# Optimization experiments

Hardware: AMD Instinct MI355X
Metric: run time of the kernel (lower is better)

The kernel has to match this reference:

```python
import jax, jax.numpy as jnp
import numpy as np

N_NODES = 100000
IN_DIM = 128
HID = 128
OUT = 64
N_EDGES = 1600000


def _glorot(key, shape):
    fan_in = shape[1]
    bound = 1.0 / np.sqrt(fan_in)
    return jax.random.uniform(key, shape, jnp.float32, -bound, bound)


def setup_inputs() -> dict:
    key = jax.random.key(0)
    ks = jax.random.split(key, 12)
    x = jax.random.normal(ks[0], (N_NODES, IN_DIM), jnp.float32)
    edge_index = jax.random.randint(ks[1], (2, N_EDGES), 0, N_NODES, jnp.int64)
    return {
        "x": x,
        "edge_index": edge_index,
        "lin_W": _glorot(ks[2], (HID, IN_DIM)),
        "lin_b": _glorot(ks[3], (1, HID))[0],
        "c1_Wl": _glorot(ks[4], (HID, HID)),
        "c1_bl": _glorot(ks[5], (1, HID))[0],
        "c1_Wr": _glorot(ks[6], (HID, HID)),
        "c2_Wl": _glorot(ks[7], (OUT, HID)),
        "c2_bl": _glorot(ks[8], (1, OUT))[0],
        "c2_Wr": _glorot(ks[9], (OUT, HID)),
    }


def _sage_conv(x, edge_index, Wl, bl, Wr):
    # PyG SAGEConv (aggr='mean'): out_i = Wl @ mean_{j in N(i)} x_j + bl + Wr @ x_i
    n = x.shape[0]
    src, dst = edge_index[0], edge_index[1]
    msg_sum = jax.ops.segment_sum(x[src], dst, num_segments=n)          # [N, d]
    deg = jax.ops.segment_sum(jnp.ones((src.shape[0],), x.dtype), dst,
                              num_segments=n)                            # [N]
    mean = msg_sum / jnp.maximum(deg, 1.0)[:, None]                      # zero-deg -> 0
    return mean @ Wl.T + bl + x @ Wr.T


def reference(x, edge_index, lin_W, lin_b, c1_Wl, c1_bl, c1_Wr, c2_Wl, c2_bl, c2_Wr):
    h = jax.nn.relu(x @ lin_W.T + lin_b)                                 # [N, HID]
    h = jax.nn.relu(_sage_conv(h, edge_index, c1_Wl, c1_bl, c1_Wr))      # [N, HID]
    h = _sage_conv(h, edge_index, c2_Wl, c2_bl, c2_Wr)                   # [N, OUT]
    return jax.nn.log_softmax(h, axis=1)
```

## Files before the change

kernel.cpp:

```cpp
#include <hip/hip_runtime.h>


#define KDIM 128
#define CH 4096
#define BSH 8
#define BCAP 8192

using bf16x8 = __attribute__((ext_vector_type(8))) short;
using f32x4  = __attribute__((ext_vector_type(4))) float;
using f32x2  = __attribute__((ext_vector_type(2))) float;

__device__ __forceinline__ unsigned short f2bf_u(float f) {
    unsigned u = __float_as_uint(f);
    u += 0x7fffu + ((u >> 16) & 1u);
    return (unsigned short)(u >> 16);
}
__device__ __forceinline__ unsigned packbf2(float a, float b) {
    return (unsigned)f2bf_u(a) | ((unsigned)f2bf_u(b) << 16);
}
__device__ __forceinline__ float bf2f(short s) {
    return __uint_as_float(((unsigned)(unsigned short)s) << 16);
}
__device__ __forceinline__ unsigned char f2fp8(float v) {
    return (unsigned char)(__builtin_amdgcn_cvt_pk_fp8_f32(v, v, 0, false) & 0xff);
}
__device__ __forceinline__ void fp8x4_acc2(unsigned uu, f32x2* a) {
    a[0] += __builtin_amdgcn_cvt_pk_f32_fp8(uu, false);
    a[1] += __builtin_amdgcn_cvt_pk_f32_fp8(uu, true);
}
__device__ __forceinline__ uint4 fp8x8_to_bf16x8(uint2 u) {
    f32x2 a0 = __builtin_amdgcn_cvt_pk_f32_fp8(u.x, false);
    f32x2 a1 = __builtin_amdgcn_cvt_pk_f32_fp8(u.x, true);
    f32x2 a2 = __builtin_amdgcn_cvt_pk_f32_fp8(u.y, false);
    f32x2 a3 = __builtin_amdgcn_cvt_pk_f32_fp8(u.y, true);
    uint4 o;
    o.x = packbf2(a0.x, a0.y); o.y = packbf2(a1.x, a1.y);
    o.z = packbf2(a2.x, a2.y); o.w = packbf2(a3.x, a3.y);
    return o;
}
__device__ __forceinline__ uint2 bf16x8_to_fp8x8(const short* p) {
    unsigned w0 = __builtin_amdgcn_cvt_pk_fp8_f32(bf2f(p[0]), bf2f(p[1]), 0, false);
    w0 = (unsigned)__builtin_amdgcn_cvt_pk_fp8_f32(bf2f(p[2]), bf2f(p[3]), (int)w0, true);
    unsigned w1 = __builtin_amdgcn_cvt_pk_fp8_f32(bf2f(p[4]), bf2f(p[5]), 0, false);
    w1 = (unsigned)__builtin_amdgcn_cvt_pk_fp8_f32(bf2f(p[6]), bf2f(p[7]), (int)w1, true);
    return uint2{w0, w1};
}

__device__ __forceinline__ void gload_lds16(const short* g, short* l) {
    __builtin_amdgcn_global_load_lds(
        (const __attribute__((address_space(1))) unsigned int*)g,
        (__attribute__((address_space(3))) unsigned int*)l, 16, 0, 0);
}

__global__ __launch_bounds__(256) void fused_front(
    const int* __restrict__ ei, int* __restrict__ hist, int E, int nwg, int NB,
    const float* __restrict__ Wc1l, const float* __restrict__ Wc1r,
    const float* __restrict__ Wc2l, const float* __restrict__ Wc2r,
    short* __restrict__ wp,
    const float* __restrict__ X, const float* __restrict__ Wlin,
    const float* __restrict__ bias, unsigned char* __restrict__ h1q, int N)
{
    __shared__ __attribute__((aligned(16))) short xa[64 * 136];
    const int bid = blockIdx.x;
    const int t = threadIdx.x;

    if (bid < nwg) {
        int* lh = (int*)xa;
        for (int b = t; b < NB; b += 256) lh[b] = 0;
        __syncthreads();
        const int e0 = bid * CH, e1 = min(E, e0 + CH);
        for (int e = e0 + t; e < e1; e += 256)
            atomicAdd(&lh[ei[E + e] >> BSH], 1);
        __syncthreads();
        for (int b = t; b < NB; b += 256) hist[b * nwg + bid] = lh[b];
        return;
    }
    if (bid < nwg + 192) {
        int idx = (bid - nwg) * 256 + t;
        const float* W; short* dst; int off, ncf;
        if (idx < 16384)      { W = Wc1l; dst = wp;         off = idx;         ncf = 8; }
        else if (idx < 32768) { W = Wc1r; dst = wp + 16384; off = idx - 16384; ncf = 8; }
        else if (idx < 40960) { W = Wc2l; dst = wp + 32768; off = idx - 32768; ncf = 4; }
        else                  { W = Wc2r; dst = wp + 40960; off = idx - 40960; ncf = 4; }
        int j    = off & 7;
        int lane = (off >> 3) & 63;
        int cf   = (off >> 9) & (ncf - 1);
        int ks   = off >> ((ncf == 8) ? 12 : 11);
        int m = cf * 16 + (lane & 15);
        int k = ks * 32 + ((lane >> 4) << 3) + j;
        dst[off] = (short)f2bf_u(W[m * KDIM + k]);
        return;
    }

    const int w = t >> 6, lane = t & 63;
    const int row0 = (bid - nwg - 192) * 64;
    const int cf0 = w * 2;

    bf16x8 bwA[4][2];
    #pragma unroll
    for (int ks = 0; ks < 4; ++ks)
        #pragma unroll
        for (int c = 0; c < 2; ++c) {
            const int m = (cf0 + c) * 16 + (lane & 15);
            const int kb = ks * 32 + ((lane >> 4) << 3);
            const float4 wa = *(const float4*)(Wlin + m * KDIM + kb);
            const float4 wb = *(const float4*)(Wlin + m * KDIM + kb + 4);
            bf16x8 r;
            r[0] = (short)f2bf_u(wa.x); r[1] = (short)f2bf_u(wa.y);
            r[2] = (short)f2bf_u(wa.z); r[3] = (short)f2bf_u(wa.w);
            r[4] = (short)f2bf_u(wb.x); r[5] = (short)f2bf_u(wb.y);
            r[6] = (short)f2bf_u(wb.z); r[7] = (short)f2bf_u(wb.w);
            bwA[ks][c] = r;
        }

    #pragma unroll
    for (int j = 0; j < 4; ++j) {
        const int sl = t + 256 * j;
        const int r = sl >> 4, s = sl & 15;
        const int gg = s ^ (r & 7);
        const int grow = min(row0 + r, N - 1);
        const float4 f0 = *(const float4*)(X + (long)grow * KDIM + gg * 8);
        const float4 f1 = *(const float4*)(X + (long)grow * KDIM + gg * 8 + 4);
        uint4 o;
        o.x = packbf2(f0.x, f0.y); o.y = packbf2(f0.z, f0.w);
        o.z = packbf2(f1.x, f1.y); o.w = packbf2(f1.z, f1.w);
        *(uint4*)(xa + r * KDIM + s * 8) = o;
    }

    f32x4 acc[4][2];
    #pragma unroll
    for (int c = 0; c < 2; ++c) {
        const float bv = bias[(cf0 + c) * 16 + (lane & 15)];
        #pragma unroll
        for (int rf = 0; rf < 4; ++rf)
            acc[rf][c] = f32x4{bv, bv, bv, bv};
    }

    __syncthreads();

    #pragma unroll
    for (int ks = 0; ks < 4; ++ks) {
        #pragma unroll
        for (int rf = 0; rf < 4; ++rf) {
            const int rl = rf * 16 + (lane & 15);
            const int s = (ks * 4 + (lane >> 4)) ^ (rl & 7);
            const bf16x8 a = *(const bf16x8*)(xa + rl * KDIM + s * 8);
            #pragma unroll
            for (int c = 0; c < 2; ++c)
                acc[rf][c] = __builtin_amdgcn_mfma_f32_16x16x32_bf16(
                    a, bwA[ks][c], acc[rf][c], 0, 0, 0);
        }
    }

    __syncthreads();
    #pragma unroll
    for (int rf = 0; rf < 4; ++rf)
        #pragma unroll
        for (int c = 0; c < 2; ++c)
            #pragma unroll
            for (int q = 0; q < 4; ++q) {
                const int r = rf * 16 + (lane >> 4) * 4 + q;
                const int col = (cf0 + c) * 16 + (lane & 15);
                xa[r * 136 + col] = (short)f2bf_u(fmaxf(acc[rf][c][q], 0.f));
            }
    __syncthreads();
    #pragma unroll
    for (int j = 0; j < 4; ++j) {
        const int sl = t + 256 * j;
        const int r = sl >> 4, ch = sl & 15;
        const int row = row0 + r;
        if (row < N)
            *(uint2*)(h1q + (long)row * KDIM + ch * 8) =
                bf16x8_to_fp8x8(xa + r * 136 + ch * 8);
    }
}


__global__ __launch_bounds__(256) void greduce(
    const int* __restrict__ in, int* __restrict__ bsum, int n)
{
    const int t = threadIdx.x;
    const int idx = blockIdx.x * 1024 + t * 4;
    int s = 0;
    if (idx + 4 <= n) {
        int4 a = *(const int4*)(in + idx);
        s = a.x + a.y + a.z + a.w;
    } else {
        #pragma unroll
        for (int k = 0; k < 4; ++k) if (idx + k < n) s += in[idx + k];
    }
    #pragma unroll
    for (int d = 1; d < 64; d <<= 1) s += __shfl_xor(s, d);
    __shared__ int ws[4];
    if ((t & 63) == 0) ws[t >> 6] = s;
    __syncthreads();
    if (t == 0) bsum[blockIdx.x] = ws[0] + ws[1] + ws[2] + ws[3];
}

__global__ __launch_bounds__(256) void scan_bsums(int* __restrict__ bsum, int nb)
{
    const int t = threadIdx.x;
    const int lane = t & 63, wid = t >> 6;
    int v = (t < nb) ? bsum[t] : 0;
    int incl = v;
    #pragma unroll
    for (int d = 1; d < 64; d <<= 1) {
        int u = __shfl_up(incl, d);
        if (lane >= d) incl += u;
    }
    __shared__ int ws[4];
    if (lane == 63) ws[wid] = incl;
    __syncthreads();
    int woff = 0;
    #pragma unroll
    for (int w = 0; w < 4; ++w) if (w < wid) woff += ws[w];
    const int excl = woff + incl - v;
    if (t <= nb) bsum[t] = excl;
}

__global__ __launch_bounds__(256) void gapply(
    int* __restrict__ io, const int* __restrict__ bsum, int n)
{
    const int t = threadIdx.x;
    const int lane = t & 63, wid = t >> 6;
    const int idx = blockIdx.x * 1024 + t * 4;
    int v[4] = {0, 0, 0, 0};
    if (idx + 4 <= n) {
        int4 a = *(const int4*)(io + idx);
        v[0] = a.x; v[1] = a.y; v[2] = a.z; v[3] = a.w;
    } else {
        #pragma unroll
        for (int k = 0; k < 4; ++k) if (idx + k < n) v[k] = io[idx + k];
    }
    const int sum = v[0] + v[1] + v[2] + v[3];
    int incl = sum;
    #pragma unroll
    for (int d = 1; d < 64; d <<= 1) {
        int u = __shfl_up(incl, d);
        if (lane >= d) incl += u;
    }
    __shared__ int ws[4];
    if (lane == 63) ws[wid] = incl;
    __syncthreads();
    int woff = 0;
    #pragma unroll
    for (int w = 0; w < 4; ++w) if (w < wid) woff += ws[w];
    int excl = bsum[blockIdx.x] + woff + (incl - sum);
    if (idx + 4 <= n) {
        int4 o;
        o.x = excl; o.y = excl + v[0]; o.z = excl + v[0] + v[1];
        o.w = excl + v[0] + v[1] + v[2];
        *(int4*)(io + idx) = o;
    } else {
        #pragma unroll
        for (int k = 0; k < 4; ++k) {
            if (idx + k < n) { io[idx + k] = excl; excl += v[k]; }
        }
    }
}

__global__ __launch_bounds__(256) void bin_scatter(
    const int* __restrict__ ei, const int* __restrict__ hist_s,
    unsigned* __restrict__ packed, int E, int nwg, int NB)
{
    __shared__ int lc[512];
    const int w = blockIdx.x, t = threadIdx.x;
    for (int b = t; b < NB; b += 256) lc[b] = hist_s[b * nwg + w];
    __syncthreads();
    const int e0 = w * CH, e1 = min(E, e0 + CH);
    for (int e = e0 + t; e < e1; e += 256) {
        const int src = ei[e];
        const int dst = ei[E + e];
        const int b = dst >> BSH;
        const int pos = atomicAdd(&lc[b], 1);
        packed[pos] = ((unsigned)(dst & 255) << 17) | (unsigned)src;
    }
}

__global__ __launch_bounds__(256) void bucket_sort(
    const unsigned* __restrict__ packed, const int* __restrict__ hist_s,
    int* __restrict__ offs, float* __restrict__ degf, int* __restrict__ perm,
    int E, int nwg, int NB, int N)
{
    __shared__ unsigned le[BCAP];
    __shared__ int lp[BCAP];
    __shared__ int lh[256], lx[256], lc[256];
    __shared__ int ws[4];
    const int b = blockIdx.x, t = threadIdx.x;
    const int bb = hist_s[b * nwg];
    const int be = (b + 1 < NB) ? hist_s[(b + 1) * nwg] : E;
    int cnt = be - bb;
    if (cnt > BCAP) cnt = BCAP;
    for (int i = t; i < cnt; i += 256) le[i] = packed[bb + i];
    lh[t] = 0;
    __syncthreads();
    for (int i = t; i < cnt; i += 256) atomicAdd(&lh[le[i] >> 17], 1);
    __syncthreads();
    const int lane = t & 63, wid = t >> 6;
    const int v = lh[t];
    int incl = v;
    #pragma unroll
    for (int d = 1; d < 64; d <<= 1) {
        int u = __shfl_up(incl, d);
        if (lane >= d) incl += u;
    }
    if (lane == 63) ws[wid] = incl;
    __syncthreads();
    int woff = 0;
    #pragma unroll
    for (int w = 0; w < 4; ++w) if (w < wid) woff += ws[w];
    const int excl = woff + incl - v;
    lx[t] = excl;
    lc[t] = excl;
    __syncthreads();
    for (int i = t; i < cnt; i += 256) {
        const unsigned p = le[i];
        const int pos = atomicAdd(&lc[p >> 17], 1);
        lp[pos] = (int)(p & 0x1FFFFu);
    }
    __syncthreads();
    for (int i = t; i < cnt; i += 256) perm[bb + i] = lp[i];
    const int node = (b << BSH) + t;
    if (node < N) {
        offs[node] = bb + lx[t];
        degf[node] = (float)v;
    }
    if (b == NB - 1 && t == 0) offs[N] = E;
}


__global__ __launch_bounds__(256) void gather_mean_128(
    const unsigned char* __restrict__ h1q, const int* __restrict__ offs,
    const int* __restrict__ perm, const float* __restrict__ degf,
    short* __restrict__ agg, int N)
{
    const int node = blockIdx.x * 16 + (threadIdx.x >> 4);
    if (node >= N) return;
    const int c = threadIdx.x & 15;
    const int b = offs[node], e = offs[node + 1];
    f32x2 acc2[4];
    #pragma unroll
    for (int q = 0; q < 4; ++q) acc2[q] = f32x2{0.f, 0.f};
    int i = b;
    for (; i + 4 <= e; i += 4) {
        const int s0 = perm[i],     s1 = perm[i + 1];
        const int s2 = perm[i + 2], s3 = perm[i + 3];
        const uint2 u0 = *(const uint2*)(h1q + (long)s0 * KDIM + c * 8);
        const uint2 u1 = *(const uint2*)(h1q + (long)s1 * KDIM + c * 8);
        const uint2 u2 = *(const uint2*)(h1q + (long)s2 * KDIM + c * 8);
        const uint2 u3 = *(const uint2*)(h1q + (long)s3 * KDIM + c * 8);
        fp8x4_acc2(u0.x, acc2 + 0);  fp8x4_acc2(u0.y, acc2 + 2);
        fp8x4_acc2(u1.x, acc2 + 0);  fp8x4_acc2(u1.y, acc2 + 2);
        fp8x4_acc2(u2.x, acc2 + 0);  fp8x4_acc2(u2.y, acc2 + 2);
        fp8x4_acc2(u3.x, acc2 + 0);  fp8x4_acc2(u3.y, acc2 + 2);
    }
    for (; i < e; ++i) {
        const uint2 u = *(const uint2*)(h1q + (long)perm[i] * KDIM + c * 8);
        fp8x4_acc2(u.x, acc2 + 0);  fp8x4_acc2(u.y, acc2 + 2);
    }
    const float inv = 1.f / fmaxf(degf[node], 1.f);
    uint4 o;
    o.x = packbf2(acc2[0].x * inv, acc2[0].y * inv);
    o.y = packbf2(acc2[1].x * inv, acc2[1].y * inv);
    o.z = packbf2(acc2[2].x * inv, acc2[2].y * inv);
    o.w = packbf2(acc2[3].x * inv, acc2[3].y * inv);
    *(uint4*)(agg + (long)node * KDIM + c * 8) = o;
}

__global__ __launch_bounds__(256) void gather_out(
    const unsigned char* __restrict__ g2q, const short* __restrict__ r2,
    const int* __restrict__ offs, const int* __restrict__ perm,
    const float* __restrict__ degf, float* __restrict__ out, int N)
{
    const int node = blockIdx.x * 32 + (threadIdx.x >> 3);
    if (node >= N) return;
    const int c = threadIdx.x & 7;
    const int b = offs[node], e = offs[node + 1];
    f32x2 acc2[4];
    #pragma unroll
    for (int q = 0; q < 4; ++q) acc2[q] = f32x2{0.f, 0.f};
    int i = b;
    for (; i + 4 <= e; i += 4) {
        const int s0 = perm[i],     s1 = perm[i + 1];
        const int s2 = perm[i + 2], s3 = perm[i + 3];
        const uint2 u0 = *(const uint2*)(g2q + (long)s0 * 64 + c * 8);
        const uint2 u1 = *(const uint2*)(g2q + (long)s1 * 64 + c * 8);
        const uint2 u2 = *(const uint2*)(g2q + (long)s2 * 64 + c * 8);
        const uint2 u3 = *(const uint2*)(g2q + (long)s3 * 64 + c * 8);
        fp8x4_acc2(u0.x, acc2 + 0);  fp8x4_acc2(u0.y, acc2 + 2);
        fp8x4_acc2(u1.x, acc2 + 0);  fp8x4_acc2(u1.y, acc2 + 2);
        fp8x4_acc2(u2.x, acc2 + 0);  fp8x4_acc2(u2.y, acc2 + 2);
        fp8x4_acc2(u3.x, acc2 + 0);  fp8x4_acc2(u3.y, acc2 + 2);
    }
    for (; i < e; ++i) {
        const uint2 u = *(const uint2*)(g2q + (long)perm[i] * 64 + c * 8);
        fp8x4_acc2(u.x, acc2 + 0);  fp8x4_acc2(u.y, acc2 + 2);
    }
    const float inv = 1.f / fmaxf(degf[node], 1.f);
    const bf16x8 rv = *(const bf16x8*)(r2 + (long)node * 64 + c * 8);
    float v[8];
    v[0] = acc2[0].x * inv + bf2f(rv[0]);
    v[1] = acc2[0].y * inv + bf2f(rv[1]);
    v[2] = acc2[1].x * inv + bf2f(rv[2]);
    v[3] = acc2[1].y * inv + bf2f(rv[3]);
    v[4] = acc2[2].x * inv + bf2f(rv[4]);
    v[5] = acc2[2].y * inv + bf2f(rv[5]);
    v[6] = acc2[3].x * inv + bf2f(rv[6]);
    v[7] = acc2[3].y * inv + bf2f(rv[7]);
    float m = v[0];
    #pragma unroll
    for (int q = 1; q < 8; ++q) m = fmaxf(m, v[q]);
    m = fmaxf(m, __shfl_xor(m, 1));
    m = fmaxf(m, __shfl_xor(m, 2));
    m = fmaxf(m, __shfl_xor(m, 4));
    float s = 0.f;
    #pragma unroll
    for (int q = 0; q < 8; ++q) s += __expf(v[q] - m);
    s += __shfl_xor(s, 1);
    s += __shfl_xor(s, 2);
    s += __shfl_xor(s, 4);
    const float L = m + __logf(s);
    float4 oa = make_float4(v[0] - L, v[1] - L, v[2] - L, v[3] - L);
    float4 ob = make_float4(v[4] - L, v[5] - L, v[6] - L, v[7] - L);
    *(float4*)(out + (long)node * 64 + c * 8) = oa;
    *(float4*)(out + (long)node * 64 + c * 8 + 4) = ob;
}

__global__ __launch_bounds__(256) void gemm_c1c2(
    const short* __restrict__ A, const unsigned char* __restrict__ h1q,
    const short* __restrict__ wpA, const short* __restrict__ wpB,
    const short* __restrict__ wpL2, const short* __restrict__ wpR2,
    const float* __restrict__ bias1, const float* __restrict__ bias2,
    unsigned char* __restrict__ g2q, short* __restrict__ r2, int N)
{
    __shared__ __attribute__((aligned(16))) short xa[64 * KDIM];
    __shared__ __attribute__((aligned(16))) short xb[64 * 136];

    const int t = threadIdx.x;
    const int w = t >> 6, lane = t & 63;
    const int row0 = blockIdx.x * 64;
    const int cf0 = w * 2;

    bf16x8 bwA[4][2], bwB[4][2];
    #pragma unroll
    for (int ks = 0; ks < 4; ++ks)
        #pragma unroll
        for (int c = 0; c < 2; ++c) {
            bwA[ks][c] = *(const bf16x8*)(wpA + (((ks * 8) + cf0 + c) * 64 + lane) * 8);
            bwB[ks][c] = *(const bf16x8*)(wpB + (((ks * 8) + cf0 + c) * 64 + lane) * 8);
        }

    #pragma unroll
    for (int ii = 0; ii < 4; ++ii) {
        const int i = w * 4 + ii;
        const int rl = i * 4 + (lane >> 4);
        const int grow = min(row0 + rl, N - 1);
        const int gs = (lane & 15) ^ (rl & 7);
        gload_lds16(A + (long)grow * KDIM + gs * 8, &xa[i * 512]);
    }
    #pragma unroll
    for (int j = 0; j < 4; ++j) {
        const int sl = t + 256 * j;
        const int r = sl >> 4, s = sl & 15;
        const int gg = s ^ (r & 7);
        const int grow = min(row0 + r, N - 1);
        const uint2 u = *(const uint2*)(h1q + (long)grow * KDIM + gg * 8);
        *(uint4*)(xb + r * KDIM + s * 8) = fp8x8_to_bf16x8(u);
    }

    f32x4 acc[4][2];
    #pragma unroll
    for (int c = 0; c < 2; ++c) {
        const float bv = bias1[(cf0 + c) * 16 + (lane & 15)];
        #pragma unroll
        for (int rf = 0; rf < 4; ++rf)
            acc[rf][c] = f32x4{bv, bv, bv, bv};
    }

    __syncthreads();

    #pragma unroll
    for (int ks = 0; ks < 4; ++ks) {
        #pragma unroll
        for (int rf = 0; rf < 4; ++rf) {
            const int rl = rf * 16 + (lane & 15);
            const int s = (ks * 4 + (lane >> 4)) ^ (rl & 7);
            const bf16x8 a = *(const bf16x8*)(xa + rl * KDIM + s * 8);
            #pragma unroll
            for (int c = 0; c < 2; ++c)
                acc[rf][c] = __builtin_amdgcn_mfma_f32_16x16x32_bf16(
                    a, bwA[ks][c], acc[rf][c], 0, 0, 0);
            const bf16x8 bb = *(const bf16x8*)(xb + rl * KDIM + s * 8);
            #pragma unroll
            for (int c = 0; c < 2; ++c)
                acc[rf][c] = __builtin_amdgcn_mfma_f32_16x16x32_bf16(
                    bb, bwB[ks][c], acc[rf][c], 0, 0, 0);
        }
    }

    __syncthreads();
    #pragma unroll
    for (int rf = 0; rf < 4; ++rf)
        #pragma unroll
        for (int c = 0; c < 2; ++c)
            #pragma unroll
            for (int q = 0; q < 4; ++q) {
                const int r = rf * 16 + (lane >> 4) * 4 + q;
                const int col = (cf0 + c) * 16 + (lane & 15);
                const int s = col >> 3;
                xa[r * KDIM + ((s ^ (r & 7)) << 3) + (col & 7)] =
                    (short)f2bf_u(fmaxf(acc[rf][c][q], 0.f));
            }

    const int side = w >> 1;
    const int cf2 = (w & 1) * 2;
    const short* wp2 = side ? wpR2 : wpL2;

    bf16x8 bw2[4][2];
    #pragma unroll
    for (int ks = 0; ks < 4; ++ks)
        #pragma unroll
        for (int c = 0; c < 2; ++c)
            bw2[ks][c] = *(const bf16x8*)(wp2 + (((ks * 4) + cf2 + c) * 64 + lane) * 8);

    f32x4 acc2[4][2];
    #pragma unroll
    for (int c = 0; c < 2; ++c) {
        const float bv = side ? bias2[(cf2 + c) * 16 + (lane & 15)] : 0.f;
        #pragma unroll
        for (int rf = 0; rf < 4; ++rf)
            acc2[rf][c] = f32x4{bv, bv, bv, bv};
    }

    __syncthreads();

    #pragma unroll
    for (int ks = 0; ks < 4; ++ks) {
        #pragma unroll
        for (int rf = 0; rf < 4; ++rf) {
            const int rl = rf * 16 + (lane & 15);
            const int s = (ks * 4 + (lane >> 4)) ^ (rl & 7);
            const bf16x8 a = *(const bf16x8*)(xa + rl * KDIM + s * 8);
            #pragma unroll
            for (int c = 0; c < 2; ++c)
                acc2[rf][c] = __builtin_amdgcn_mfma_f32_16x16x32_bf16(
                    a, bw2[ks][c], acc2[rf][c], 0, 0, 0);
        }
    }

    {
        short* et = xb + (side ? 64 * 68 : 0);
        #pragma unroll
        for (int rf = 0; rf < 4; ++rf)
            #pragma unroll
            for (int c = 0; c < 2; ++c)
                #pragma unroll
                for (int q = 0; q < 4; ++q) {
                    const int r = rf * 16 + (lane >> 4) * 4 + q;
                    const int col = (cf2 + c) * 16 + (lane & 15);
                    et[r * 68 + col] = (short)f2bf_u(acc2[rf][c][q]);
                }
    }
    __syncthreads();
    #pragma unroll
    for (int j = 0; j < 2; ++j) {
        const int sl = t + 256 * j;
        const int r = sl >> 3, ch = sl & 7;
        const int row = row0 + r;
        if (row < N)
            *(uint2*)(g2q + (long)row * 64 + ch * 8) =
                bf16x8_to_fp8x8(xb + r * 68 + ch * 8);
    }
    #pragma unroll
    for (int j = 0; j < 2; ++j) {
        const int sl = t + 256 * j;
        const int r = sl >> 3, ch = sl & 7;
        const int row = row0 + r;
        if (row < N)
            *(uint4*)(r2 + (long)row * 64 + ch * 8) =
                *(const uint4*)(xb + 64 * 68 + r * 68 + ch * 8);
    }
}

extern "C" void kernel_launch(void* const* d_in, const int* in_sizes, int n_in,
                              void* d_out, int out_size, void* d_ws, size_t ws_size,
                              hipStream_t stream) {
    const float* x     = (const float*)d_in[0];
    const int*   ei    = (const int*)d_in[1];
    const float* lin_W = (const float*)d_in[2];
    const float* lin_b = (const float*)d_in[3];
    const float* c1_Wl = (const float*)d_in[4];
    const float* c1_bl = (const float*)d_in[5];
    const float* c1_Wr = (const float*)d_in[6];
    const float* c2_Wl = (const float*)d_in[7];
    const float* c2_bl = (const float*)d_in[8];
    const float* c2_Wr = (const float*)d_in[9];
    float* out = (float*)d_out;

    const int N = in_sizes[0] / KDIM;
    const int E = in_sizes[1] / 2;

    short* aggb = (short*)d_ws;
    short* r2   = aggb + (size_t)N * KDIM;
    unsigned char* h1q = (unsigned char*)(r2 + (size_t)N * 64);
    unsigned char* g2q = h1q + (size_t)N * KDIM;
    short* wp   = (short*)(g2q + (size_t)N * 64);
    float* degf = (float*)(wp + 49152);
    int* offs   = (int*)(degf + N);
    const int nwg = (E + CH - 1) / CH;
    const int NB  = (N + 255) >> BSH;
    int* hist   = offs + (N + 1);
    int* bsum   = hist + NB * nwg;
    unsigned* packed = (unsigned*)(bsum + 256);
    int* perm   = (int*)(packed + E);

    const int nb = (N + 63) / 64;
    const int nh = NB * nwg;
    const int nsb = (nh + 1023) / 1024;

    fused_front<<<nwg + 192 + nb, 256, 0, stream>>>(
        ei, hist, E, nwg, NB,
        c1_Wl, c1_Wr, c2_Wl, c2_Wr, wp,
        x, lin_W, lin_b, h1q, N);

    greduce<<<nsb, 256, 0, stream>>>(hist, bsum, nh);
    scan_bsums<<<1, 256, 0, stream>>>(bsum, nsb);
    gapply<<<nsb, 256, 0, stream>>>(hist, bsum, nh);
    bin_scatter<<<nwg, 256, 0, stream>>>(ei, hist, packed, E, nwg, NB);
    bucket_sort<<<NB, 256, 0, stream>>>(packed, hist, offs, degf, perm, E, nwg, NB, N);

    gather_mean_128<<<(N + 15) / 16, 256, 0, stream>>>(h1q, offs, perm, degf, aggb, N);

    gemm_c1c2<<<nb, 256, 0, stream>>>(
        aggb, h1q, wp, wp + 16384, wp + 32768, wp + 40960,
        c1_bl, c2_bl, g2q, r2, N);

    gather_out<<<(N + 31) / 32, 256, 0, stream>>>(g2q, r2, offs, perm, degf, out, N);
}
```

Baseline: 141.6 us.

## Fuse layer-1 neighbor mean gather into the conv GEMM kernel

Removes the separate gather_mean_128 kernel and its bf16 aggregate buffer; the GEMM block now computes each of its 64 rows' neighbor mean directly from fp8 features into swizzled LDS, with 4 threads per node each covering 32 channels. This drops a global write/read of the N x 128 aggregate and one launch. In exchange each thread holds 32 float accumulators and does fewer but wider loads with less memory-level parallelism per node. The GEMM kernel's occupancy may drop from the higher register use.

```diff
diff --git a/kernel.cpp b/kernel.cpp
--- a/kernel.cpp
+++ b/kernel.cpp
@@ -44,12 +44,6 @@
     unsigned w1 = __builtin_amdgcn_cvt_pk_fp8_f32(bf2f(p[4]), bf2f(p[5]), 0, false);
     w1 = (unsigned)__builtin_amdgcn_cvt_pk_fp8_f32(bf2f(p[6]), bf2f(p[7]), (int)w1, true);
     return uint2{w0, w1};
-}
-
-__device__ __forceinline__ void gload_lds16(const short* g, short* l) {
-    __builtin_amdgcn_global_load_lds(
-        (const __attribute__((address_space(1))) unsigned int*)g,
-        (__attribute__((address_space(3))) unsigned int*)l, 16, 0, 0);
 }
 
 __global__ __launch_bounds__(256) void fused_front(
@@ -328,45 +322,6 @@
     if (b == NB - 1 && t == 0) offs[N] = E;
 }
 
-
-__global__ __launch_bounds__(256) void gather_mean_128(
-    const unsigned char* __restrict__ h1q, const int* __restrict__ offs,
-    const int* __restrict__ perm, const float* __restrict__ degf,
-    short* __restrict__ agg, int N)
-{
-    const int node = blockIdx.x * 16 + (threadIdx.x >> 4);
-    if (node >= N) return;
-    const int c = threadIdx.x & 15;
-    const int b = offs[node], e = offs[node + 1];
-    f32x2 acc2[4];
-    #pragma unroll
-    for (int q = 0; q < 4; ++q) acc2[q] = f32x2{0.f, 0.f};
-    int i = b;
-    for (; i + 4 <= e; i += 4) {
-        const int s0 = perm[i],     s1 = perm[i + 1];
-        const int s2 = perm[i + 2], s3 = perm[i + 3];
-        const uint2 u0 = *(const uint2*)(h1q + (long)s0 * KDIM + c * 8);
-        const uint2 u1 = *(const uint2*)(h1q + (long)s1 * KDIM + c * 8);
-        const uint2 u2 = *(const uint2*)(h1q + (long)s2 * KDIM + c * 8);
-        const uint2 u3 = *(const uint2*)(h1q + (long)s3 * KDIM + c * 8);
-        fp8x4_acc2(u0.x, acc2 + 0);  fp8x4_acc2(u0.y, acc2 + 2);
-        fp8x4_acc2(u1.x, acc2 + 0);  fp8x4_acc2(u1.y, acc2 + 2);
-        fp8x4_acc2(u2.x, acc2 + 0);  fp8x4_acc2(u2.y, acc2 + 2);
-        fp8x4_acc2(u3.x, acc2 + 0);  fp8x4_acc2(u3.y, acc2 + 2);
-    }
-    for (; i < e; ++i) {
-        const uint2 u = *(const uint2*)(h1q + (long)perm[i] * KDIM + c * 8);
-        fp8x4_acc2(u.x, acc2 + 0);  fp8x4_acc2(u.y, acc2 + 2);
-    }
-    const float inv = 1.f / fmaxf(degf[node], 1.f);
-    uint4 o;
-    o.x = packbf2(acc2[0].x * inv, acc2[0].y * inv);
-    o.y = packbf2(acc2[1].x * inv, acc2[1].y * inv);
-    o.z = packbf2(acc2[2].x * inv, acc2[2].y * inv);
-    o.w = packbf2(acc2[3].x * inv, acc2[3].y * inv);
-    *(uint4*)(agg + (long)node * KDIM + c * 8) = o;
-}
-
 __global__ __launch_bounds__(256) void gather_out(
     const unsigned char* __restrict__ g2q, const short* __restrict__ r2,
     const int* __restrict__ offs, const int* __restrict__ perm,
@@ -427,7 +382,8 @@
 }
 
 __global__ __launch_bounds__(256) void gemm_c1c2(
-    const short* __restrict__ A, const unsigned char* __restrict__ h1q,
+    const unsigned char* __restrict__ h1q, const int* __restrict__ offs,
+    const int* __restrict__ perm, const float* __restrict__ degf,
     const short* __restrict__ wpA, const short* __restrict__ wpB,
     const short* __restrict__ wpL2, const short* __restrict__ wpR2,
     const float* __restrict__ bias1, const float* __restrict__ bias2,
@@ -439,25 +395,54 @@
     const int t = threadIdx.x;
     const int w = t >> 6, lane = t & 63;
     const int row0 = blockIdx.x * 64;
-    const int cf0 = w * 2;
-
-    bf16x8 bwA[4][2], bwB[4][2];
-    #pragma unroll
-    for (int ks = 0; ks < 4; ++ks)
-        #pragma unroll
-        for (int c = 0; c < 2; ++c) {
-            bwA[ks][c] = *(const bf16x8*)(wpA + (((ks * 8) + cf0 + c) * 64 + lane) * 8);
-            bwB[ks][c] = *(const bf16x8*)(wpB + (((ks * 8) + cf0 + c) * 64 + lane) * 8);
-        }
-
-    #pragma unroll
-    for (int ii = 0; ii < 4; ++ii) {
-        const int i = w * 4 + ii;
-        const int rl = i * 4 + (lane >> 4);
-        const int grow = min(row0 + rl, N - 1);
-        const int gs = (lane & 15) ^ (rl & 7);
-        gload_lds16(A + (long)grow * KDIM + gs * 8, &xa[i * 512]);
-    }
+
+    {
+        const int r = t >> 2;
+        const int qc = t & 3;
+        const int node = min(row0 + r, N - 1);
+        const int b = offs[node], e = offs[node + 1];
+        f32x2 a0[16];
+        #pragma unroll
+        for (int q = 0; q < 16; ++q) a0[q] = f32x2{0.f, 0.f};
+        const unsigned char* hp = h1q + qc * 32;
+        int i = b;
+        for (; i + 2 <= e; i += 2) {
+            const int s0 = perm[i], s1 = perm[i + 1];
+            const uint4 u0 = *(const uint4*)(hp + (long)s0 * KDIM);
+            const uint4 v0 = *(const uint4*)(hp + (long)s0 * KDIM + 16);
+            const uint4 u1 = *(const uint4*)(hp + (long)s1 * KDIM);
+            const uint4 v1 = *(const uint4*)(hp + (long)s1 * KDIM + 16);
+            fp8x4_acc2(u0.x, a0 + 0);  fp8x4_acc2(u0.y, a0 + 2);
+            fp8x4_acc2(u0.z, a0 + 4);  fp8x4_acc2(u0.w, a0 + 6);
+            fp8x4_acc2(v0.x, a0 + 8);  fp8x4_acc2(v0.y, a0 + 10);
+            fp8x4_acc2(v0.z, a0 + 12); fp8x4_acc2(v0.w, a0 + 14);
+            fp8x4_acc2(u1.x, a0 + 0);  fp8x4_acc2(u1.y, a0 + 2);
+            fp8x4_acc2(u1.z, a0 + 4);  fp8x4_acc2(u1.w, a0 + 6);
+            fp8x4_acc2(v1.x, a0 + 8);  fp8x4_acc2(v1.y, a0 + 10);
+            fp8x4_acc2(v1.z, a0 + 12); fp8x4_acc2(v1.w, a0 + 14);
+        }
+        if (i < e) {
+            const int s0 = perm[i];
+            const uint4 u0 = *(const uint4*)(hp + (long)s0 * KDIM);
+            const uint4 v0 = *(const uint4*)(hp + (long)s0 * KDIM + 16);
+            fp8x4_acc2(u0.x, a0 + 0);  fp8x4_acc2(u0.y, a0 + 2);
+            fp8x4_acc2(u0.z, a0 + 4);  fp8x4_acc2(u0.w, a0 + 6);
+            fp8x4_acc2(v0.x, a0 + 8);  fp8x4_acc2(v0.y, a0 + 10);
+            fp8x4_acc2(v0.z, a0 + 12); fp8x4_acc2(v0.w, a0 + 14);
+        }
+        const float inv = 1.f / fmaxf(degf[node], 1.f);
+        #pragma unroll
+        for (int j = 0; j < 4; ++j) {
+            const int slot = (qc * 4 + j) ^ (r & 7);
+            uint4 o;
+            o.x = packbf2(a0[4 * j + 0].x * inv, a0[4 * j + 0].y * inv);
+            o.y = packbf2(a0[4 * j + 1].x * inv, a0[4 * j + 1].y * inv);
+            o.z = packbf2(a0[4 * j + 2].x * inv, a0[4 * j + 2].y * inv);
+            o.w = packbf2(a0[4 * j + 3].x * inv, a0[4 * j + 3].y * inv);
+            *(uint4*)(xa + r * KDIM + slot * 8) = o;
+        }
+    }
+
     #pragma unroll
     for (int j = 0; j < 4; ++j) {
         const int sl = t + 256 * j;
@@ -467,6 +452,16 @@
         const uint2 u = *(const uint2*)(h1q + (long)grow * KDIM + gg * 8);
         *(uint4*)(xb + r * KDIM + s * 8) = fp8x8_to_bf16x8(u);
     }
+
+    const int cf0 = w * 2;
+    bf16x8 bwA[4][2], bwB[4][2];
+    #pragma unroll
+    for (int ks = 0; ks < 4; ++ks)
+        #pragma unroll
+        for (int c = 0; c < 2; ++c) {
+            bwA[ks][c] = *(const bf16x8*)(wpA + (((ks * 8) + cf0 + c) * 64 + lane) * 8);
+            bwB[ks][c] = *(const bf16x8*)(wpB + (((ks * 8) + cf0 + c) * 64 + lane) * 8);
+        }
 
     f32x4 acc[4][2];
     #pragma unroll
@@ -600,8 +595,7 @@
     const int N = in_sizes[0] / KDIM;
     const int E = in_sizes[1] / 2;
 
-    short* aggb = (short*)d_ws;
-    short* r2   = aggb + (size_t)N * KDIM;
+    short* r2   = (short*)d_ws;
     unsigned char* h1q = (unsigned char*)(r2 + (size_t)N * 64);
     unsigned char* g2q = h1q + (size_t)N * KDIM;
     short* wp   = (short*)(g2q + (size_t)N * 64);
@@ -629,10 +623,9 @@
     bin_scatter<<<nwg, 256, 0, stream>>>(ei, hist, packed, E, nwg, NB);
     bucket_sort<<<NB, 256, 0, stream>>>(packed, hist, offs, degf, perm, E, nwg, NB, N);
 
-    gather_mean_128<<<(N + 15) / 16, 256, 0, stream>>>(h1q, offs, perm, degf, aggb, N);
-
     gemm_c1c2<<<nb, 256, 0, stream>>>(
-        aggb, h1q, wp, wp + 16384, wp + 32768, wp + 40960,
+        h1q, offs, perm, degf,
+        wp, wp + 16384, wp + 32768, wp + 40960,
         c1_bl, c2_bl, g2q, r2, N);
 
     gather_out<<<(N + 31) / 32, 256, 0, stream>>>(g2q, r2, offs, perm, degf, out, N);
```

Result: no change. 139.5 us (-1.5%).
